# Performance work log

Hardware: AMD Instinct MI355X
Metric: run time of the kernel (lower is better)

## Reference

```python
import jax, jax.numpy as jnp
import numpy as np

N_NODES = 100000


def setup_inputs() -> dict:
    key = jax.random.key(0)
    ks = jax.random.split(key, 4)
    x = jax.random.normal(ks[0], (N_NODES, 64), dtype=jnp.float32)
    edge_index = jax.random.randint(ks[1], (2, 1600000), 0, N_NODES, dtype=jnp.int64)
    # Glorot-ish scaled weights
    W1 = jax.random.normal(ks[2], (64, 64), dtype=jnp.float32) * (1.0 / np.sqrt(64))
    b1 = jnp.zeros((64,), dtype=jnp.float32)
    W2 = jax.random.normal(ks[3], (64, 19), dtype=jnp.float32) * (1.0 / np.sqrt(64))
    b2 = jnp.zeros((19,), dtype=jnp.float32)
    return {"x": x, "edge_index": edge_index, "W1": W1, "b1": b1, "W2": W2, "b2": b2}


def _gcn_norm(edge_index, num_nodes, dtype):
    # PyG gcn_norm: add self-loops (fill_value=1, improved=False), then
    # norm = deg^-1/2[src] * deg^-1/2[dst] with deg computed over destination.
    loops = jnp.arange(num_nodes, dtype=edge_index.dtype)
    src = jnp.concatenate([edge_index[0], loops])
    dst = jnp.concatenate([edge_index[1], loops])
    deg = jax.ops.segment_sum(jnp.ones_like(dst, dtype=dtype), dst, num_segments=num_nodes)
    dinv = jax.lax.rsqrt(deg)  # deg >= 1 thanks to self-loops
    norm = dinv[src] * dinv[dst]  # [E + N]
    return src, dst, norm


def _gcn_conv(h, src, dst, norm, W, b, num_nodes):
    hw = h @ W                                  # dense transform [N, d_out]
    msg = norm[:, None] * hw[src]               # gather + edge scaling [E+N, d_out]
    out = jax.ops.segment_sum(msg, dst, num_segments=num_nodes)  # scatter-add
    return out + b


def reference(x, edge_index, W1, b1, W2, b2):
    n = x.shape[0]
    src, dst, norm = _gcn_norm(edge_index, n, x.dtype)
    h = jax.nn.relu(_gcn_conv(x, src, dst, norm, W1, b1, n))
    # dropout is identity in eval mode (training=False)
    return _gcn_conv(h, src, dst, norm, W2, b2, n)
```

## Files before the change

kernel.cpp:

```cpp
#include <hip/hip_runtime.h>

#define TPB 256
#define BSH 5
#define BNODES 32
#define CAP 1024
#define EPB 4096
#define NBMAX 3200


__global__ void k_hist1(const int* __restrict__ dst, int* __restrict__ hist,
                        int nb, int E) {
    __shared__ int sh[NBMAX];
    int tid = threadIdx.x, blk = blockIdx.x;
    for (int i = tid; i < nb; i += TPB) sh[i] = 0;
    __syncthreads();
    int e0 = blk * EPB;
    for (int i = tid; i < EPB; i += TPB) {
        int e = e0 + i;
        if (e < E) atomicAdd(&sh[dst[e] >> BSH], 1);
    }
    __syncthreads();
    int* hrow = hist + (size_t)blk * nb;
    for (int i = tid; i < nb; i += TPB) hrow[i] = sh[i];
}

__global__ void k_scanoff(const int* __restrict__ hist, int* __restrict__ offs,
                          int* __restrict__ bcnt, int nblk, int nb) {
    int t = blockIdx.x * TPB + threadIdx.x;
    int b = t >> 3, s = t & 7;
    if (b >= nb) return;
    int nps = (nblk + 7) >> 3;
    int sum = 0;
    for (int q = 0; q < nps; ++q) {
        int blk = q * 8 + s;
        if (blk < nblk) sum += hist[(size_t)blk * nb + b];
    }
    int v = sum;
#pragma unroll
    for (int o = 1; o < 8; o <<= 1) {
        int u = __shfl_up(v, o, 8);
        if (s >= o) v += u;
    }
    int total = __shfl(v, 7, 8);
    if (s == 0) bcnt[b] = total;
    int off = b * CAP + (v - sum);
    for (int q = 0; q < nps; ++q) {
        int blk = q * 8 + s;
        if (blk < nblk) {
            offs[(size_t)blk * nb + b] = off;
            off += hist[(size_t)blk * nb + b];
        }
    }
}

__global__ void k_scatter(const int* __restrict__ src, const int* __restrict__ dst,
                          const int* __restrict__ offs, unsigned* __restrict__ ebuf,
                          int nb, int E) {
    __shared__ int cur[NBMAX];
    int tid = threadIdx.x, blk = blockIdx.x;
    const int* orow = offs + (size_t)blk * nb;
    for (int i = tid; i < nb; i += TPB) cur[i] = orow[i];
    __syncthreads();
    int e0 = blk * EPB;
    for (int i = tid; i < EPB; i += TPB) {
        int e = e0 + i;
        if (e < E) {
            int d = dst[e];
            int pos = atomicAdd(&cur[d >> BSH], 1);
            ebuf[pos] = ((unsigned)src[e] << BSH) | (unsigned)(d & (BNODES - 1));
        }
    }
}

__global__ void k_bcsr(const int* __restrict__ bcnt, const unsigned* __restrict__ ebuf,
                       int* __restrict__ csr, int* __restrict__ node_beg,
                       int* __restrict__ degi, float* __restrict__ dinv, int nb, int n) {
    __shared__ unsigned se[4][CAP];
    __shared__ int scnt[4][BNODES];
    __shared__ int sexc[4][BNODES];
    __shared__ int srnk[4][BNODES];
    int wv = threadIdx.x >> 6, lane = threadIdx.x & 63;
    int b = blockIdx.x * 4 + wv;
    bool act = (b < nb);
    if (lane < BNODES) { scnt[wv][lane] = 0; srnk[wv][lane] = 0; }
    __syncthreads();
    int cnt = 0;
    if (act) {
        cnt = bcnt[b];
        if (cnt > CAP) cnt = CAP;
        const unsigned* p = &ebuf[(size_t)b * CAP];
        for (int k = lane; k < cnt; k += 64) {
            unsigned pk = p[k];
            se[wv][k] = pk;
            atomicAdd(&scnt[wv][pk & (BNODES - 1)], 1);
        }
    }
    __syncthreads();
    if (act && lane < BNODES) {
        int dg = scnt[wv][lane];
        int v = dg;
#pragma unroll
        for (int off = 1; off < BNODES; off <<= 1) {
            int t = __shfl_up(v, off, BNODES);
            if (lane >= off) v += t;
        }
        int excl = v - dg;
        sexc[wv][lane] = excl;
        int node = b * BNODES + lane;
        if (node < n) {
            degi[node] = dg;
            node_beg[node] = b * CAP + excl;
            dinv[node] = rsqrtf((float)dg + 1.0f);
        }
    }
    __syncthreads();
    if (act) {
        int* csrb = csr + (size_t)b * CAP;
        for (int k = lane; k < cnt; k += 64) {
            unsigned pk = se[wv][k];
            int dl = pk & (BNODES - 1);
            int r = atomicAdd(&srnk[wv][dl], 1);
            csrb[sexc[wv][dl] + r] = (int)(pk >> BSH);
        }
    }
}


__global__ void k_xw64v(const float* __restrict__ x, const float* __restrict__ W,
                        const float* __restrict__ dinv, _Float16* __restrict__ g, int n) {
    __shared__ float Ws[64 * 64];
    __shared__ float xsT[64 * 64];
    int tid = threadIdx.x;
    int row0 = blockIdx.x * 64;
    for (int i = tid; i < 1024; i += TPB)
        reinterpret_cast<float4*>(Ws)[i] = reinterpret_cast<const float4*>(W)[i];
    {
        int rl = tid >> 2, cq = (tid & 3) * 16;
        int row = row0 + rl;
#pragma unroll
        for (int j4 = 0; j4 < 4; ++j4) {
            float4 v = make_float4(0.f, 0.f, 0.f, 0.f);
            if (row < n) v = *reinterpret_cast<const float4*>(x + (size_t)row * 64 + cq + j4 * 4);
            xsT[(cq + j4 * 4 + 0) * 64 + rl] = v.x;
            xsT[(cq + j4 * 4 + 1) * 64 + rl] = v.y;
            xsT[(cq + j4 * 4 + 2) * 64 + rl] = v.z;
            xsT[(cq + j4 * 4 + 3) * 64 + rl] = v.w;
        }
    }
    __syncthreads();
    int c4 = (tid & 15) * 4, rq = (tid >> 4) * 4;
    float acc[4][4] = {};
#pragma unroll 4
    for (int k = 0; k < 64; ++k) {
        float4 wv = *reinterpret_cast<const float4*>(Ws + k * 64 + c4);
        float4 xv = *reinterpret_cast<const float4*>(xsT + k * 64 + rq);
        const float* wp = (const float*)&wv;
        const float* xp = (const float*)&xv;
#pragma unroll
        for (int i = 0; i < 4; ++i)
#pragma unroll
            for (int j = 0; j < 4; ++j) acc[i][j] += xp[i] * wp[j];
    }
#pragma unroll
    for (int i = 0; i < 4; ++i) {
        int row = row0 + rq + i;
        if (row < n) {
            float dv = dinv[row];
            _Float16 o[4];
#pragma unroll
            for (int j = 0; j < 4; ++j) o[j] = (_Float16)(dv * acc[i][j]);
            *reinterpret_cast<ushort4*>(g + (size_t)row * 64 + c4) =
                *reinterpret_cast<const ushort4*>(o);
        }
    }
}

__global__ void k_xw19v(const _Float16* __restrict__ h, const float* __restrict__ W,
                        const float* __restrict__ dinv, _Float16* __restrict__ g2, int n) {
    __shared__ float Ws[64 * 32];
    __shared__ float xsT[64 * 32];
    int tid = threadIdx.x;
    int row0 = blockIdx.x * 32;
    for (int i = tid; i < 64 * 32; i += TPB) {
        int k = i >> 5, c = i & 31;
        Ws[i] = (c < 19) ? W[k * 19 + c] : 0.f;
    }
    {
        int rl = tid >> 3, sq = tid & 7;
        int row = row0 + rl;
        if (row < n) {
            uint4 v = *(reinterpret_cast<const uint4*>(h + (size_t)row * 64) + sq);
            const _Float16* f = (const _Float16*)&v;
#pragma unroll
            for (int j = 0; j < 8; ++j) xsT[(sq * 8 + j) * 32 + rl] = (float)f[j];
        } else {
#pragma unroll
            for (int j = 0; j < 8; ++j) xsT[(sq * 8 + j) * 32 + rl] = 0.f;
        }
    }
    __syncthreads();
    int c = tid & 31, rg = (tid >> 5) * 4;
    float acc[4] = {};
#pragma unroll 4
    for (int k = 0; k < 64; ++k) {
        float wv = Ws[k * 32 + c];
        float4 xv = *reinterpret_cast<const float4*>(xsT + k * 32 + rg);
        const float* xp = (const float*)&xv;
#pragma unroll
        for (int i = 0; i < 4; ++i) acc[i] += xp[i] * wv;
    }
    if (c < 19) {
#pragma unroll
        for (int i = 0; i < 4; ++i) {
            int row = row0 + rg + i;
            if (row < n) g2[(size_t)row * 19 + c] = (_Float16)(dinv[row] * acc[i]);
        }
    }
}


__global__ void k_gath64h(const int* __restrict__ node_beg, const int* __restrict__ degi,
                          const int* __restrict__ csr, const float* __restrict__ dinv,
                          const _Float16* __restrict__ g, const float* __restrict__ b1,
                          _Float16* __restrict__ h, int n, int halfsel) {
    int node = blockIdx.x * 4 + (threadIdx.x >> 6);
    if (node >= n) return;
    int lane = threadIdx.x & 63;
    int eidx = lane >> 2, fch = lane & 3;
    int beg = node_beg[node], cnt = degi[node];
    const uint4* gb = (const uint4*)g;
    int coff = halfsel * 4 + fch;
    float acc[8];
#pragma unroll
    for (int j = 0; j < 8; ++j) acc[j] = 0.f;
    for (int base = 0; base < cnt; base += 16) {
        int k = base + eidx;
        if (k < cnt) {
            int row = csr[beg + k];
            uint4 v = gb[(size_t)row * 8 + coff];
            const _Float16* f = (const _Float16*)&v;
#pragma unroll
            for (int j = 0; j < 8; ++j) acc[j] += (float)f[j];
        }
    }
#pragma unroll
    for (int m = 4; m < 64; m <<= 1) {
#pragma unroll
        for (int j = 0; j < 8; ++j) acc[j] += __shfl_xor(acc[j], m);
    }
    if (eidx == 0) {
        uint4 v = gb[(size_t)node * 8 + coff];
        const _Float16* f = (const _Float16*)&v;
        float dv = dinv[node];
        int c0 = halfsel * 32 + fch * 8;
        _Float16 outv[8];
#pragma unroll
        for (int j = 0; j < 8; ++j) {
            float val = dv * (acc[j] + (float)f[j]) + b1[c0 + j];
            outv[j] = (_Float16)fmaxf(val, 0.f);
        }
        *reinterpret_cast<uint4*>(h + (size_t)node * 64 + c0) =
            *reinterpret_cast<const uint4*>(outv);
    }
}

__global__ void k_gath19(const int* __restrict__ node_beg, const int* __restrict__ degi,
                         const int* __restrict__ csr, const float* __restrict__ dinv,
                         const _Float16* __restrict__ g2, const float* __restrict__ b2,
                         float* __restrict__ out, int n) {
    int node = blockIdx.x * 8 + (threadIdx.x >> 5);
    if (node >= n) return;
    int c = threadIdx.x & 31;
    if (c >= 19) return;
    int beg = node_beg[node], cnt = degi[node];
    float a0 = (float)g2[(size_t)node * 19 + c];
    float a1 = 0.f, a2 = 0.f, a3 = 0.f;
    float a4 = 0.f, a5 = 0.f, a6 = 0.f, a7 = 0.f;
    int k = 0;
    for (; k + 7 < cnt; k += 8) {
        int s0 = csr[beg + k];
        int s1 = csr[beg + k + 1];
        int s2 = csr[beg + k + 2];
        int s3 = csr[beg + k + 3];
        int s4 = csr[beg + k + 4];
        int s5 = csr[beg + k + 5];
        int s6 = csr[beg + k + 6];
        int s7 = csr[beg + k + 7];
        a0 += (float)g2[(size_t)s0 * 19 + c];
        a1 += (float)g2[(size_t)s1 * 19 + c];
        a2 += (float)g2[(size_t)s2 * 19 + c];
        a3 += (float)g2[(size_t)s3 * 19 + c];
        a4 += (float)g2[(size_t)s4 * 19 + c];
        a5 += (float)g2[(size_t)s5 * 19 + c];
        a6 += (float)g2[(size_t)s6 * 19 + c];
        a7 += (float)g2[(size_t)s7 * 19 + c];
    }
    for (; k < cnt; ++k) a1 += (float)g2[(size_t)csr[beg + k] * 19 + c];
    float s = ((a0 + a1) + (a2 + a3)) + ((a4 + a5) + (a6 + a7));
    out[(size_t)node * 19 + c] = dinv[node] * s + b2[c];
}


extern "C" void kernel_launch(void* const* d_in, const int* in_sizes, int n_in,
                              void* d_out, int out_size, void* d_ws, size_t ws_size,
                              hipStream_t stream) {
    const float* x  = (const float*)d_in[0];
    const int*   ei = (const int*)d_in[1];
    const float* W1 = (const float*)d_in[2];
    const float* b1 = (const float*)d_in[3];
    const float* W2 = (const float*)d_in[4];
    const float* b2 = (const float*)d_in[5];
    float* out = (float*)d_out;

    int N = in_sizes[0] / 64;
    int E = in_sizes[1] / 2;
    const int* src = ei;
    const int* dst = ei + E;

    int NB = (N + BNODES - 1) >> BSH;
    int NBLK = (E + EPB - 1) / EPB;

    char* w = (char*)d_ws;
    int* bcnt      = (int*)w;      w += (size_t)NB * 4;
    int* degi      = (int*)w;      w += (size_t)N * 4;
    int* node_beg  = (int*)w;      w += (size_t)N * 4;
    float* dinv    = (float*)w;    w += (size_t)N * 4;
    w = (char*)(((size_t)w + 63) & ~(size_t)63);
    char* regionA  = w;
    size_t histB   = (size_t)NBLK * NB * 4;
    size_t csrB    = (size_t)NB * CAP * 4;
    size_t regA    = (histB * 2 > csrB) ? histB * 2 : csrB;
    int* hist      = (int*)regionA;
    int* offs      = (int*)(regionA + histB);
    int* csr       = (int*)regionA;
    w += regA;
    unsigned* ebuf = (unsigned*)w; w += (size_t)NB * CAP * 4;
    _Float16* g1   = (_Float16*)w; w += (size_t)N * 64 * 2;
    _Float16* h    = (_Float16*)w; w += (size_t)N * 64 * 2;
    _Float16* g2   = g1;

    k_hist1   <<<NBLK, TPB, 0, stream>>>(dst, hist, NB, E);
    k_scanoff <<<(NB * 8 + TPB - 1) / TPB, TPB, 0, stream>>>(hist, offs, bcnt, NBLK, NB);
    k_scatter <<<NBLK, TPB, 0, stream>>>(src, dst, offs, ebuf, NB, E);
    k_bcsr    <<<(NB + 3) / 4, TPB, 0, stream>>>(bcnt, ebuf, csr, node_beg, degi, dinv, NB, N);

    k_xw64v   <<<(N + 63) / 64, TPB, 0, stream>>>(x, W1, dinv, g1, N);
    k_gath64h <<<(N + 3) / 4, TPB, 0, stream>>>(node_beg, degi, csr, dinv, g1, b1, h, N, 0);
    k_gath64h <<<(N + 3) / 4, TPB, 0, stream>>>(node_beg, degi, csr, dinv, g1, b1, h, N, 1);

    k_xw19v   <<<(N + 31) / 32, TPB, 0, stream>>>(h, W2, dinv, g2, N);
    k_gath19  <<<(N + 7) / 8, TPB, 0, stream>>>(node_beg, degi, csr, dinv, g2, b2, out, N);
}
```

Before: 230.0 us.

## Merge half-feature gathers into one interleaved launch with 2x edge unroll

Replaces the two sequential half-channel gather launches with one launch whose block index interleaves the two feature halves for the same group of nodes, so both halves run close together in time and share the CSR index reads and cache locality. The inner edge loop now processes two edges per lane per iteration, issuing two independent gathers to increase memory-level parallelism. This adds some register pressure and wasted predicated loads for low-degree nodes.

```diff
diff --git a/kernel.cpp b/kernel.cpp
--- a/kernel.cpp
+++ b/kernel.cpp
@@ -219,29 +219,34 @@
 }
 
 
-__global__ void k_gath64h(const int* __restrict__ node_beg, const int* __restrict__ degi,
+__global__ void k_gath64x(const int* __restrict__ node_beg, const int* __restrict__ degi,
                           const int* __restrict__ csr, const float* __restrict__ dinv,
                           const _Float16* __restrict__ g, const float* __restrict__ b1,
-                          _Float16* __restrict__ h, int n, int halfsel) {
-    int node = blockIdx.x * 4 + (threadIdx.x >> 6);
+                          _Float16* __restrict__ h, int n) {
+    int bid = blockIdx.x;
+    int half = (bid >> 2) & 1;
+    int gidx = (bid >> 3) * 4 + (bid & 3);
+    int node = gidx * 4 + (threadIdx.x >> 6);
     if (node >= n) return;
     int lane = threadIdx.x & 63;
     int eidx = lane >> 2, fch = lane & 3;
     int beg = node_beg[node], cnt = degi[node];
     const uint4* gb = (const uint4*)g;
-    int coff = halfsel * 4 + fch;
+    int coff = half * 4 + fch;
     float acc[8];
 #pragma unroll
     for (int j = 0; j < 8; ++j) acc[j] = 0.f;
-    for (int base = 0; base < cnt; base += 16) {
-        int k = base + eidx;
-        if (k < cnt) {
-            int row = csr[beg + k];
-            uint4 v = gb[(size_t)row * 8 + coff];
-            const _Float16* f = (const _Float16*)&v;
-#pragma unroll
-            for (int j = 0; j < 8; ++j) acc[j] += (float)f[j];
-        }
+    for (int base = 0; base < cnt; base += 32) {
+        int ka = base + eidx, kb = base + 16 + eidx;
+        bool va = (ka < cnt), vb = (kb < cnt);
+        int ra = va ? csr[beg + ka] : 0;
+        int rb = vb ? csr[beg + kb] : 0;
+        uint4 A = va ? gb[(size_t)ra * 8 + coff] : make_uint4(0, 0, 0, 0);
+        uint4 B = vb ? gb[(size_t)rb * 8 + coff] : make_uint4(0, 0, 0, 0);
+        const _Float16* fa = (const _Float16*)&A;
+        const _Float16* fb = (const _Float16*)&B;
+#pragma unroll
+        for (int j = 0; j < 8; ++j) acc[j] += (float)fa[j] + (float)fb[j];
     }
 #pragma unroll
     for (int m = 4; m < 64; m <<= 1) {
@@ -252,7 +257,7 @@
         uint4 v = gb[(size_t)node * 8 + coff];
         const _Float16* f = (const _Float16*)&v;
         float dv = dinv[node];
-        int c0 = halfsel * 32 + fch * 8;
+        int c0 = half * 32 + fch * 8;
         _Float16 outv[8];
 #pragma unroll
         for (int j = 0; j < 8; ++j) {
@@ -345,8 +350,11 @@
     k_bcsr    <<<(NB + 3) / 4, TPB, 0, stream>>>(bcnt, ebuf, csr, node_beg, degi, dinv, NB, N);
 
     k_xw64v   <<<(N + 63) / 64, TPB, 0, stream>>>(x, W1, dinv, g1, N);
-    k_gath64h <<<(N + 3) / 4, TPB, 0, stream>>>(node_beg, degi, csr, dinv, g1, b1, h, N, 0);
-    k_gath64h <<<(N + 3) / 4, TPB, 0, stream>>>(node_beg, degi, csr, dinv, g1, b1, h, N, 1);
+    {
+        int ng = (N + 3) / 4;
+        int grid = 8 * ((ng + 3) / 4);
+        k_gath64x<<<grid, TPB, 0, stream>>>(node_beg, degi, csr, dinv, g1, b1, h, N);
+    }
 
     k_xw19v   <<<(N + 31) / 32, TPB, 0, stream>>>(h, W2, dinv, g2, N);
     k_gath19  <<<(N + 7) / 8, TPB, 0, stream>>>(node_beg, degi, csr, dinv, g2, b2, out, N);
```

Measured after the change: 226.0 us. No clear change (-1.7%).
